# Kernel optimization log

Measured on AMD Instinct MI355X. Metric: run time of the kernel, lower is better.

The kernel has to match this reference:

```python
import jax, jax.numpy as jnp
import numpy as np

VOCAB = 128000
DIM = 1024
B, S = 8, 2048


def setup_inputs() -> dict:
    key = jax.random.key(0)
    k1, k2, k3, k4 = jax.random.split(key, 4)
    input = jax.random.randint(k1, (B, S), 0, VOCAB, dtype=jnp.int64)
    # uint8-valued codes stored as int32 (values in [0, 256))
    qweight = jax.random.randint(k2, (VOCAB, DIM), 0, 256, dtype=jnp.int32)
    scales = jax.random.uniform(k3, (VOCAB,), dtype=jnp.float32) * 0.02
    zeros = jax.random.uniform(k4, (VOCAB,), dtype=jnp.float32) * 255.0
    return {"input": input, "qweight": qweight, "scales": scales, "zeros": zeros}


def reference(input, qweight, scales, zeros):
    # Faithful to the torch module: dequantize the FULL table, then gather rows.
    # weight[r, d] = (q[r, d] - zero[r]) * scale[r]
    weight = (qweight.astype(jnp.float32) - zeros[:, None]) * scales[:, None]  # [V, D]
    return weight[input]  # [B, S, D] gather (padding_idx=None -> plain embedding lookup)
```

## Files before the change

### kernel.cpp

```cpp
#include <hip/hip_runtime.h>


constexpr int DIM = 1024;

__global__ __launch_bounds__(256) void qembed_kernel(
    const int*   __restrict__ input,
    const int*   __restrict__ qweight,
    const float* __restrict__ scales,
    const float* __restrict__ zeros,
    float*       __restrict__ out,
    int ntok)
{
    const int tok = blockIdx.x;
    if (tok >= ntok) return;

    const int row = input[tok];
    const float scale = scales[row];
    const float zero  = zeros[row];

    const int4* qrow = reinterpret_cast<const int4*>(qweight + (long long)row * DIM);
    float4*     orow = reinterpret_cast<float4*>(out + (long long)tok * DIM);

    const int t = threadIdx.x;
    int4 q = qrow[t];
    float4 o;
    o.x = ((float)q.x - zero) * scale;
    o.y = ((float)q.y - zero) * scale;
    o.z = ((float)q.z - zero) * scale;
    o.w = ((float)q.w - zero) * scale;
    orow[t] = o;
}

extern "C" void kernel_launch(void* const* d_in, const int* in_sizes, int n_in,
                              void* d_out, int out_size, void* d_ws, size_t ws_size,
                              hipStream_t stream) {
    const int*   input   = (const int*)d_in[0];
    const int*   qweight = (const int*)d_in[1];
    const float* scales  = (const float*)d_in[2];
    const float* zeros   = (const float*)d_in[3];
    float*       out     = (float*)d_out;

    const int ntok = in_sizes[0];
    dim3 grid(ntok);
    dim3 block(256);
    qembed_kernel<<<grid, block, 0, stream>>>(input, qweight, scales, zeros, out, ntok);
}
```

Before: 25.75 us.

## Process one token per wavefront with four vector loads and nontemporal accesses

Each 64-lane wavefront now handles a whole embedding row, with four 16-byte loads per lane, and each block covers four tokens, so the grid shrinks fourfold. Loads and stores use nontemporal builtins so the streamed rows and the output bypass or lightly use the caches. The aim is fewer blocks, more bytes in flight per thread and less cache pollution. The cost is more registers per thread, and nontemporal stores could behave differently on this memory subsystem.

```diff
diff --git a/kernel.cpp b/kernel.cpp
--- a/kernel.cpp
+++ b/kernel.cpp
@@ -2,6 +2,9 @@
 
 
 constexpr int DIM = 1024;
+
+typedef int   int4v   __attribute__((ext_vector_type(4)));
+typedef float float4v __attribute__((ext_vector_type(4)));
 
 __global__ __launch_bounds__(256) void qembed_kernel(
     const int*   __restrict__ input,
@@ -11,24 +14,35 @@
     float*       __restrict__ out,
     int ntok)
 {
-    const int tok = blockIdx.x;
+    const int tok  = blockIdx.x * 4 + (threadIdx.x >> 6);
+    const int lane = threadIdx.x & 63;
     if (tok >= ntok) return;
 
     const int row = input[tok];
     const float scale = scales[row];
     const float zero  = zeros[row];
 
-    const int4* qrow = reinterpret_cast<const int4*>(qweight + (long long)row * DIM);
-    float4*     orow = reinterpret_cast<float4*>(out + (long long)tok * DIM);
+    const int4v*  qrow = reinterpret_cast<const int4v*>(qweight + (size_t)row * DIM);
+    float4v*      orow = reinterpret_cast<float4v*>(out + (size_t)tok * DIM);
 
-    const int t = threadIdx.x;
-    int4 q = qrow[t];
-    float4 o;
-    o.x = ((float)q.x - zero) * scale;
-    o.y = ((float)q.y - zero) * scale;
-    o.z = ((float)q.z - zero) * scale;
-    o.w = ((float)q.w - zero) * scale;
-    orow[t] = o;
+    int4v q0 = __builtin_nontemporal_load(qrow + lane);
+    int4v q1 = __builtin_nontemporal_load(qrow + lane + 64);
+    int4v q2 = __builtin_nontemporal_load(qrow + lane + 128);
+    int4v q3 = __builtin_nontemporal_load(qrow + lane + 192);
+
+    float4v o0, o1, o2, o3;
+    #pragma unroll
+    for (int j = 0; j < 4; ++j) {
+        o0[j] = ((float)q0[j] - zero) * scale;
+        o1[j] = ((float)q1[j] - zero) * scale;
+        o2[j] = ((float)q2[j] - zero) * scale;
+        o3[j] = ((float)q3[j] - zero) * scale;
+    }
+
+    __builtin_nontemporal_store(o0, orow + lane);
+    __builtin_nontemporal_store(o1, orow + lane + 64);
+    __builtin_nontemporal_store(o2, orow + lane + 128);
+    __builtin_nontemporal_store(o3, orow + lane + 192);
 }
 
 extern "C" void kernel_launch(void* const* d_in, const int* in_sizes, int n_in,
@@ -41,7 +55,7 @@
     float*       out     = (float*)d_out;
 
     const int ntok = in_sizes[0];
-    dim3 grid(ntok);
+    dim3 grid((ntok + 3) / 4);
     dim3 block(256);
     qembed_kernel<<<grid, block, 0, stream>>>(input, qweight, scales, zeros, out, ntok);
 }
```

Result: slower. 27.80 us (+8.0%).
